# Kernel tuning notes

Measured on AMD Instinct MI355X. Metric: run time of the kernel, lower is better.

Reference implementation:

```python
import jax, jax.numpy as jnp
import numpy as np

IN_DIM = 128
HID = 128
NUM_CLASSES = 10
N_NODES = 100000
N_EDGES = 1600000
NUM_GRAPHS = 128


def setup_inputs() -> dict:
    key = jax.random.key(0)
    ks = jax.random.split(key, 12)
    X = jax.random.normal(ks[0], (N_NODES, IN_DIM), dtype=jnp.float32)
    EI = jax.random.randint(ks[1], (2, N_EDGES), 0, N_NODES, dtype=jnp.int64)
    batch = jnp.sort(jax.random.randint(ks[2], (N_NODES,), 0, NUM_GRAPHS, dtype=jnp.int64))
    s_in = 1.0 / np.sqrt(IN_DIM)
    s_h = 1.0 / np.sqrt(HID)
    s_m = 1.0 / np.sqrt(2 * HID)
    params = {
        'W1': jax.random.uniform(ks[3], (IN_DIM, HID), jnp.float32, -s_in, s_in),
        'b1': jnp.zeros((HID,), jnp.float32),
        'W2': jax.random.uniform(ks[4], (HID, HID), jnp.float32, -s_h, s_h),
        'b2': jnp.zeros((HID,), jnp.float32),
        'W3': jax.random.uniform(ks[5], (HID, HID), jnp.float32, -s_h, s_h),
        'b3': jnp.zeros((HID,), jnp.float32),
        'Wm1': jax.random.uniform(ks[6], (2 * HID, HID), jnp.float32, -s_m, s_m),
        'bm1': jnp.zeros((HID,), jnp.float32),
        'Wm2': jax.random.uniform(ks[7], (HID, NUM_CLASSES), jnp.float32, -s_h, s_h),
        'bm2': jnp.zeros((NUM_CLASSES,), jnp.float32),
    }
    return dict(X=X, EI=EI, batch=batch, num_graphs=NUM_GRAPHS, **params)


def _gcn_norm(EI, n):
    # add self loops, compute D^{-1/2}[row] * D^{-1/2}[col]
    loops = jnp.arange(n, dtype=EI.dtype)
    row = jnp.concatenate([EI[0], loops])
    col = jnp.concatenate([EI[1], loops])
    deg = jax.ops.segment_sum(jnp.ones_like(row, dtype=jnp.float32), row, num_segments=n)
    dis = (deg + 1e-12) ** -0.5
    norm = dis[row] * dis[col]
    return row, col, norm


def _gcn_layer(x, row, col, norm, W, b):
    h = x @ W + b                       # [N, out]
    msg = h[col] * norm[:, None]        # gather + scale  [E+N, out]
    return jax.ops.segment_sum(msg, row, num_segments=x.shape[0])  # scatter-add


def _pool_mean_max(x, batch, num_graphs):
    s = jax.ops.segment_sum(x, batch, num_segments=num_graphs)
    cnt = jax.ops.segment_sum(jnp.ones((x.shape[0],), x.dtype), batch, num_segments=num_graphs)
    mean = s / (cnt[:, None] + 1e-12)
    mx = jax.ops.segment_max(x, batch, num_segments=num_graphs)
    return jnp.concatenate([mean, mx], axis=1)


def reference(X, EI, batch, num_graphs, W1, b1, W2, b2, W3, b3, Wm1, bm1, Wm2, bm2):
    n = X.shape[0]
    row, col, norm = _gcn_norm(EI, n)
    x = jax.nn.relu(_gcn_layer(X, row, col, norm, W1, b1))
    x = jax.nn.relu(_gcn_layer(x, row, col, norm, W2, b2))
    x = jax.nn.relu(_gcn_layer(x, row, col, norm, W3, b3))
    g = _pool_mean_max(x, batch, num_graphs)
    h = jax.nn.relu(g @ Wm1 + bm1)
    return h @ Wm2 + bm2
```

## Files before the change

kernel.cpp:

```cpp
#include <hip/hip_runtime.h>
#include <hip/hip_fp16.h>
#include <cstdint>
#include <cstddef>

#define DIM 128
#define NG 128
#define NCLS 10
#define PSLICE 8
#define CPAD 64
#define NOWN 256
#define RPB 391
#define NPBLK 1024
#define OCAP 16
#define OVCAP 65536

typedef _Float16 f16;
typedef __attribute__((ext_vector_type(8))) _Float16 f16x8;
typedef __attribute__((ext_vector_type(4))) float f32x4;


__global__ __launch_bounds__(256) void k_part(
    const int* __restrict__ rw, const int* __restrict__ cl, int E,
    unsigned* __restrict__ buckets, int* __restrict__ bcnt,
    unsigned long long* __restrict__ ovf, int* __restrict__ ovfn) {
  __shared__ int lcnt[NOWN];
  if (threadIdx.x < NOWN) lcnt[threadIdx.x] = 0;
  __syncthreads();
  int b = blockIdx.x;
  int C = (((E + NPBLK - 1) / NPBLK + 3) & ~3);
  int s = b * C;
  int e = s + C;
  if (e > E) e = E;
  auto put = [&](int r, int c) {
    int o = (unsigned)r / RPB;
    int li = r - o * RPB;
    int sl = atomicAdd(&lcnt[o], 1);
    if (sl < OCAP) {
      buckets[((size_t)o * NPBLK + b) * OCAP + sl] =
          ((unsigned)li << 17) | (unsigned)c;
    } else {
      int oi = atomicAdd(ovfn, 1);
      if (oi < OVCAP)
        ovf[oi] = ((unsigned long long)(unsigned)r << 32) | (unsigned)c;
    }
  };
  for (int i = s + (int)threadIdx.x * 4; i < e; i += 1024) {
    if (i + 3 < e) {
      int4 r4 = *(const int4*)(rw + i);
      int4 c4 = *(const int4*)(cl + i);
      put(r4.x, c4.x);
      put(r4.y, c4.y);
      put(r4.z, c4.z);
      put(r4.w, c4.w);
    } else {
      for (int j = i; j < e; ++j) put(rw[j], cl[j]);
    }
  }
  __syncthreads();
  if (threadIdx.x < NOWN) {
    int v = lcnt[threadIdx.x];
    bcnt[threadIdx.x * NPBLK + b] = v < OCAP ? v : OCAP;
  }
}

__global__ __launch_bounds__(256) void k_place(
    const unsigned* __restrict__ buckets, const int* __restrict__ bcnt,
    const unsigned long long* __restrict__ ovf, const int* __restrict__ ovfn,
    int* __restrict__ cnt, float* __restrict__ dis, int* __restrict__ csrc,
    int N) {
  extern __shared__ int sm[];
  int* lcnt = sm;
  int* csr = sm + ((RPB + 3) & ~3);
  int o = blockIdx.x;
  int r0 = o * RPB;
  int rows = N - r0;
  if (rows > RPB) rows = RPB;
  if (rows <= 0) return;
  for (int i = threadIdx.x; i < rows; i += 256) lcnt[i] = 0;
  __syncthreads();
  const int* bc = bcnt + o * NPBLK;
  const unsigned* bp = buckets + (size_t)o * NPBLK * OCAP;
  for (int j = (int)threadIdx.x; j < NPBLK * OCAP; j += 256) {
    int seg = j >> 4;
    int pos = j & 15;
    if (pos < bc[seg]) {
      unsigned ent = bp[j];
      int li = (int)(ent >> 17);
      int c = (int)(ent & 0x1ffffu);
      int sl = atomicAdd(&lcnt[li], 1);
      if (sl < CPAD) csr[(li << 6) + sl] = c;
    }
  }
  int nov = *ovfn;
  if (nov > OVCAP) nov = OVCAP;
  for (int j = (int)threadIdx.x; j < nov; j += 256) {
    unsigned long long ent = ovf[j];
    int r = (int)(unsigned)(ent >> 32);
    int li = r - r0;
    if (li >= 0 && li < rows) {
      int c = (int)(unsigned)(ent & 0xffffffffu);
      int sl = atomicAdd(&lcnt[li], 1);
      if (sl < CPAD) csr[(li << 6) + sl] = c;
    }
  }
  __syncthreads();
  uint4* dst = (uint4*)(csrc + ((size_t)r0 << 6));
  const uint4* src = (const uint4*)csr;
  int n4 = rows * 16;
  for (int j = (int)threadIdx.x; j < n4; j += 256) dst[j] = src[j];
  for (int i = threadIdx.x; i < rows; i += 256) {
    int v = lcnt[i];
    cnt[r0 + i] = v;
    dis[r0 + i] = rsqrtf((float)(v + 1));
  }
}

__global__ void k_wt(const float* __restrict__ W1, const float* __restrict__ W2,
                     const float* __restrict__ W3, __half* __restrict__ Wt1,
                     __half* __restrict__ Wt2, __half* __restrict__ Wt3) {
  int gi = blockIdx.x * 256 + threadIdx.x;
  int m = gi / (DIM * DIM);
  int i = gi % (DIM * DIM);
  const float* W = (m == 0) ? W1 : (m == 1) ? W2 : W3;
  __half* Wt = (m == 0) ? Wt1 : (m == 1) ? Wt2 : Wt3;
  int k = i >> 7, c = i & 127;
  Wt[(size_t)c * DIM + k] = __float2half(W[(size_t)k * DIM + c]);
}


template <int FP32IN>
__global__ __launch_bounds__(256, 3) void k_gemm(
    const void* __restrict__ Ain, const __half* __restrict__ Wt,
    const float* __restrict__ bias, const float* __restrict__ dis,
    __half* __restrict__ Hh, int N) {
  int t = threadIdx.x;
  int lane = t & 63;
  int wv = t >> 6;
  int l15 = lane & 15, lg = lane >> 4;
  int cb = (wv & 1) * 64;

  f16x8 bfr[4][4];
#pragma unroll
  for (int ct = 0; ct < 4; ++ct) {
    int c = cb + ct * 16 + l15;
    const f16* wp = (const f16*)Wt + (size_t)c * DIM + lg * 8;
#pragma unroll
    for (int ks = 0; ks < 4; ++ks) bfr[ks][ct] = *(const f16x8*)(wp + ks * 32);
  }
  float bv[4];
#pragma unroll
  for (int ct = 0; ct < 4; ++ct) bv[ct] = bias[cb + ct * 16 + l15];

  const int nt2 = (N + 31) / 32;
  for (int t2 = blockIdx.x; t2 < nt2; t2 += gridDim.x) {
    int row0 = t2 * 32 + (wv >> 1) * 16;
    int rA = row0 + l15;
    if (rA > N - 1) rA = N - 1;
    f16x8 afr[4];
    if constexpr (FP32IN) {
      const float* ap = (const float*)Ain + (size_t)rA * DIM + lg * 8;
#pragma unroll
      for (int ks = 0; ks < 4; ++ks) {
        float4 v0 = *(const float4*)(ap + ks * 32);
        float4 v1 = *(const float4*)(ap + ks * 32 + 4);
        f16x8 a;
        a[0] = (f16)v0.x; a[1] = (f16)v0.y; a[2] = (f16)v0.z; a[3] = (f16)v0.w;
        a[4] = (f16)v1.x; a[5] = (f16)v1.y; a[6] = (f16)v1.z; a[7] = (f16)v1.w;
        afr[ks] = a;
      }
    } else {
      const f16* ap = (const f16*)Ain + (size_t)rA * DIM + lg * 8;
#pragma unroll
      for (int ks = 0; ks < 4; ++ks) afr[ks] = *(const f16x8*)(ap + ks * 32);
    }

    f32x4 acc[4];
#pragma unroll
    for (int ct = 0; ct < 4; ++ct) acc[ct] = (f32x4){0.f, 0.f, 0.f, 0.f};
#pragma unroll
    for (int ks = 0; ks < 4; ++ks)
#pragma unroll
      for (int ct = 0; ct < 4; ++ct)
        acc[ct] = __builtin_amdgcn_mfma_f32_16x16x32_f16(afr[ks], bfr[ks][ct], acc[ct], 0, 0, 0);

#pragma unroll
    for (int j = 0; j < 4; ++j) {
      int r = row0 + lg * 4 + j;
      if (r < N) {
        float dr = dis[r];
#pragma unroll
        for (int ct = 0; ct < 4; ++ct) {
          float o = (acc[ct][j] + bv[ct]) * dr;
          Hh[(size_t)r * DIM + cb + ct * 16 + l15] = __float2half(o);
        }
      }
    }
  }
}


__global__ __launch_bounds__(256) void k_agg(
    const __half* __restrict__ Hh, __half* __restrict__ Ah,
    const int* __restrict__ csrc, const int* __restrict__ cntA,
    const float* __restrict__ dis, int N) {
  int wave = (int)(((size_t)blockIdx.x * blockDim.x + threadIdx.x) >> 6);
  int lane = threadIdx.x & 63;
  int g = lane >> 4;
  int q = lane & 15;
  int r = wave * 4 + g;
  if (r >= N) return;
  int cnt = cntA[r];
  if (cnt > CPAD) cnt = CPAD;
  float dr = dis[r];
  const int* cp = csrc + ((size_t)r << 6);
  const f16* hb = (const f16*)Hh + q * 8;

  float4 aA0 = {0,0,0,0}, aA1 = {0,0,0,0};
  float4 aB0 = {0,0,0,0}, aB1 = {0,0,0,0};
  float4 aC0 = {0,0,0,0}, aC1 = {0,0,0,0};
  float4 aD0 = {0,0,0,0}, aD1 = {0,0,0,0};

#define ACC8(u, x0, x1)                                                   \
  {                                                                       \
    float2 f_;                                                            \
    f_ = __half22float2(*reinterpret_cast<const __half2*>(&(u).x));       \
    x0.x += f_.x; x0.y += f_.y;                                           \
    f_ = __half22float2(*reinterpret_cast<const __half2*>(&(u).y));       \
    x0.z += f_.x; x0.w += f_.y;                                           \
    f_ = __half22float2(*reinterpret_cast<const __half2*>(&(u).z));       \
    x1.x += f_.x; x1.y += f_.y;                                           \
    f_ = __half22float2(*reinterpret_cast<const __half2*>(&(u).w));       \
    x1.z += f_.x; x1.w += f_.y;                                           \
  }

  int i = 0;
  for (; i + 7 < cnt; i += 8) {
    int4 ci0 = *(const int4*)(cp + i);
    int4 ci1 = *(const int4*)(cp + i + 4);
    uint4 u0 = *(const uint4*)(hb + (size_t)ci0.x * DIM);
    uint4 u1 = *(const uint4*)(hb + (size_t)ci0.y * DIM);
    uint4 u2 = *(const uint4*)(hb + (size_t)ci0.z * DIM);
    uint4 u3 = *(const uint4*)(hb + (size_t)ci0.w * DIM);
    uint4 u4 = *(const uint4*)(hb + (size_t)ci1.x * DIM);
    uint4 u5 = *(const uint4*)(hb + (size_t)ci1.y * DIM);
    uint4 u6 = *(const uint4*)(hb + (size_t)ci1.z * DIM);
    uint4 u7 = *(const uint4*)(hb + (size_t)ci1.w * DIM);
    ACC8(u0, aA0, aA1);
    ACC8(u1, aB0, aB1);
    ACC8(u2, aC0, aC1);
    ACC8(u3, aD0, aD1);
    ACC8(u4, aA0, aA1);
    ACC8(u5, aB0, aB1);
    ACC8(u6, aC0, aC1);
    ACC8(u7, aD0, aD1);
  }
  for (; i < cnt; ++i) {
    int c0 = cp[i];
    uint4 u0 = *(const uint4*)(hb + (size_t)c0 * DIM);
    ACC8(u0, aA0, aA1);
  }
  {
    uint4 us = *(const uint4*)(hb + (size_t)r * DIM);
    ACC8(us, aA0, aA1);
  }
#undef ACC8
  float4 s0, s1;
  s0.x = (aA0.x + aB0.x) + (aC0.x + aD0.x);
  s0.y = (aA0.y + aB0.y) + (aC0.y + aD0.y);
  s0.z = (aA0.z + aB0.z) + (aC0.z + aD0.z);
  s0.w = (aA0.w + aB0.w) + (aC0.w + aD0.w);
  s1.x = (aA1.x + aB1.x) + (aC1.x + aD1.x);
  s1.y = (aA1.y + aB1.y) + (aC1.y + aD1.y);
  s1.z = (aA1.z + aB1.z) + (aC1.z + aD1.z);
  s1.w = (aA1.w + aB1.w) + (aC1.w + aD1.w);
  float o0 = fmaxf(dr * s0.x, 0.f), o1 = fmaxf(dr * s0.y, 0.f);
  float o2 = fmaxf(dr * s0.z, 0.f), o3 = fmaxf(dr * s0.w, 0.f);
  float o4 = fmaxf(dr * s1.x, 0.f), o5 = fmaxf(dr * s1.y, 0.f);
  float o6 = fmaxf(dr * s1.z, 0.f), o7 = fmaxf(dr * s1.w, 0.f);
  __half2 p0 = __floats2half2_rn(o0, o1);
  __half2 p1 = __floats2half2_rn(o2, o3);
  __half2 p2 = __floats2half2_rn(o4, o5);
  __half2 p3 = __floats2half2_rn(o6, o7);
  uint4 u;
  u.x = *(unsigned int*)&p0;
  u.y = *(unsigned int*)&p1;
  u.z = *(unsigned int*)&p2;
  u.w = *(unsigned int*)&p3;
  *(uint4*)((f16*)Ah + (size_t)r * DIM + q * 8) = u;
}


__global__ void k_bounds(const int* __restrict__ batch, int N, int G,
                         int* __restrict__ starts) {
  int i = blockIdx.x * blockDim.x + threadIdx.x;
  if (i >= N) return;
  int b = batch[i];
  int pb = (i == 0) ? -1 : batch[i - 1];
  for (int g = pb + 1; g <= b; ++g) starts[g] = i;
  if (i == N - 1) {
    for (int g = b + 1; g <= G; ++g) starts[g] = N;
  }
}

__global__ void k_pool1(const __half* __restrict__ A, const int* __restrict__ starts,
                        float* __restrict__ part) {
  int g = blockIdx.x / PSLICE, sl = blockIdx.x % PSLICE;
  int c = threadIdx.x;
  int s = starts[g], e = starts[g + 1];
  int len = e - s;
  int ns = s + (len * sl) / PSLICE;
  int ne = s + (len * (sl + 1)) / PSLICE;
  float sum = 0.f, mx = -INFINITY;
  for (int n = ns; n < ne; ++n) {
    float v = __half2float(A[(size_t)n * DIM + c]);
    sum += v;
    mx = fmaxf(mx, v);
  }
  part[((size_t)(g * PSLICE + sl) * 2 + 0) * DIM + c] = sum;
  part[((size_t)(g * PSLICE + sl) * 2 + 1) * DIM + c] = mx;
}

__global__ void k_pool2(const float* __restrict__ part, const int* __restrict__ starts,
                        float* __restrict__ GF) {
  int g = blockIdx.x;
  int c = threadIdx.x;
  float sum = 0.f, mx = -INFINITY;
  for (int sl = 0; sl < PSLICE; ++sl) {
    sum += part[((size_t)(g * PSLICE + sl) * 2 + 0) * DIM + c];
    mx = fmaxf(mx, part[((size_t)(g * PSLICE + sl) * 2 + 1) * DIM + c]);
  }
  int cntg = starts[g + 1] - starts[g];
  GF[(size_t)g * 256 + c] = sum / ((float)cntg + 1e-12f);
  GF[(size_t)g * 256 + 128 + c] = mx;
}


__global__ void k_mlp1(const float* __restrict__ GF, const float* __restrict__ Wm1,
                       const float* __restrict__ bm1, float* __restrict__ H1) {
  __shared__ float gs[256];
  int g = blockIdx.x, j = threadIdx.x;
  gs[j] = GF[(size_t)g * 256 + j];
  gs[j + 128] = GF[(size_t)g * 256 + 128 + j];
  __syncthreads();
  float acc = bm1[j];
#pragma unroll 8
  for (int k = 0; k < 256; ++k) acc = fmaf(gs[k], Wm1[k * DIM + j], acc);
  H1[(size_t)g * DIM + j] = fmaxf(acc, 0.f);
}

__global__ void k_mlp2(const float* __restrict__ H1, const float* __restrict__ Wm2,
                       const float* __restrict__ bm2, float* __restrict__ out) {
  __shared__ float hs[DIM];
  int g = blockIdx.x, j = threadIdx.x;
  hs[j] = H1[(size_t)g * DIM + j];
  hs[j + 64] = H1[(size_t)g * DIM + j + 64];
  __syncthreads();
  if (j < NCLS) {
    float acc = bm2[j];
#pragma unroll 8
    for (int k = 0; k < DIM; ++k) acc = fmaf(hs[k], Wm2[k * NCLS + j], acc);
    out[(size_t)g * NCLS + j] = acc;
  }
}


static inline size_t al256(size_t x) { return (x + 255) & ~(size_t)255; }

extern "C" void kernel_launch(void* const* d_in, const int* in_sizes, int n_in,
                              void* d_out, int out_size, void* d_ws, size_t ws_size,
                              hipStream_t stream) {
  const float* X = (const float*)d_in[0];
  const int* EI = (const int*)d_in[1];
  const int* batch = (const int*)d_in[2];
  const float* W1 = (const float*)d_in[4];
  const float* b1 = (const float*)d_in[5];
  const float* W2 = (const float*)d_in[6];
  const float* b2 = (const float*)d_in[7];
  const float* W3 = (const float*)d_in[8];
  const float* b3 = (const float*)d_in[9];
  const float* Wm1 = (const float*)d_in[10];
  const float* bm1 = (const float*)d_in[11];
  const float* Wm2 = (const float*)d_in[12];
  const float* bm2 = (const float*)d_in[13];
  float* OUT = (float*)d_out;

  const int N = in_sizes[0] / DIM;
  const int E = in_sizes[1] / 2;
  const int G = NG;

  const int* EI_row = EI;
  const int* EI_col = EI + E;

  char* p = (char*)d_ws;
  size_t off = 0;
  auto take = [&](size_t bytes) { void* r = p + off; off = al256(off + bytes); return r; };

  int* cnt = (int*)take((size_t)N * 4);
  int* bcnt = (int*)take((size_t)NOWN * NPBLK * 4);
  int* ovfn = (int*)take(256);
  unsigned long long* ovf = (unsigned long long*)take((size_t)OVCAP * 8);
  int* starts = (int*)take((size_t)(G + 1) * 4);
  float* dis = (float*)take((size_t)N * 4);
  int* csrc = (int*)take((size_t)N * CPAD * 4);
  unsigned* buckets = (unsigned*)take((size_t)NOWN * NPBLK * OCAP * 4);
  __half* Hh = (__half*)take((size_t)N * DIM * 2);
  __half* Ah = (__half*)take((size_t)N * DIM * 2);
  __half* Wt1 = (__half*)take((size_t)DIM * DIM * 2);
  __half* Wt2 = (__half*)take((size_t)DIM * DIM * 2);
  __half* Wt3 = (__half*)take((size_t)DIM * DIM * 2);
  float* part = (float*)take((size_t)G * PSLICE * 2 * DIM * 4);
  float* GF = (float*)take((size_t)G * 256 * 4);
  float* H1 = (float*)take((size_t)G * DIM * 4);
  (void)ws_size; (void)n_in; (void)out_size;

  hipMemsetAsync(ovfn, 0, 4, stream);

  k_part<<<NPBLK, 256, 0, stream>>>(EI_row, EI_col, E, buckets, bcnt, ovf, ovfn);
  const int placeLds = ((RPB + 3) & ~3) * 4 + RPB * 64 * 4;
  k_place<<<NOWN, 256, placeLds, stream>>>(buckets, bcnt, ovf, ovfn, cnt, dis, csrc, N);
  k_wt<<<192, 256, 0, stream>>>(W1, W2, W3, Wt1, Wt2, Wt3);

  const int aggBlocks = (N * 16 + 255) / 256;

  k_gemm<1><<<512, 256, 0, stream>>>(X, Wt1, b1, dis, Hh, N);
  k_agg<<<aggBlocks, 256, 0, stream>>>(Hh, Ah, csrc, cnt, dis, N);
  k_gemm<0><<<512, 256, 0, stream>>>(Ah, Wt2, b2, dis, Hh, N);
  k_agg<<<aggBlocks, 256, 0, stream>>>(Hh, Ah, csrc, cnt, dis, N);
  k_gemm<0><<<512, 256, 0, stream>>>(Ah, Wt3, b3, dis, Hh, N);
  k_agg<<<aggBlocks, 256, 0, stream>>>(Hh, Ah, csrc, cnt, dis, N);

  k_bounds<<<(N + 255) / 256, 256, 0, stream>>>(batch, N, G, starts);
  k_pool1<<<G * PSLICE, DIM, 0, stream>>>(Ah, starts, part);
  k_pool2<<<G, DIM, 0, stream>>>(part, starts, GF);

  k_mlp1<<<G, DIM, 0, stream>>>(GF, Wm1, bm1, H1);
  k_mlp2<<<G, 64, 0, stream>>>(H1, Wm2, bm2, OUT);
}
```

Measured before the change: 387.7 us.

## Split feature matrix into per-XCD column panels for L2-local aggregation

Stores the hidden feature matrices as 8 column panels of 16 halfs each. Each aggregation block reads its XCC ID from a hardware register and processes only the panel for its XCD, so each XCD's L2 caches a 3.2MB panel instead of the full matrix. Rows are taken from per-XCD atomic work counters through a persistent grid of 1024 blocks. The GEMM and pooling kernels are changed to read and write the panel layout. Correctness depends on every XCD getting enough blocks to drain its counter, and each gather is now only 8 bytes per lane, so memory transactions are narrower.

```diff
diff --git a/kernel.cpp b/kernel.cpp
--- a/kernel.cpp
+++ b/kernel.cpp
@@ -13,6 +13,8 @@
 #define NPBLK 1024
 #define OCAP 16
 #define OVCAP 65536
+#define NXCD 8
+#define XCCID_IMM ((31 << 11) | (0 << 6) | 20)
 
 typedef _Float16 f16;
 typedef __attribute__((ext_vector_type(8))) _Float16 f16x8;
@@ -132,12 +134,14 @@
 __global__ __launch_bounds__(256, 3) void k_gemm(
     const void* __restrict__ Ain, const __half* __restrict__ Wt,
     const float* __restrict__ bias, const float* __restrict__ dis,
-    __half* __restrict__ Hh, int N) {
+    __half* __restrict__ Hp, int N) {
+  const size_t PSTR = (size_t)N * 16;
   int t = threadIdx.x;
   int lane = t & 63;
   int wv = t >> 6;
   int l15 = lane & 15, lg = lane >> 4;
   int cb = (wv & 1) * 64;
+  int pb = (wv & 1) * 4;
 
   f16x8 bfr[4][4];
 #pragma unroll
@@ -169,9 +173,13 @@
         afr[ks] = a;
       }
     } else {
-      const f16* ap = (const f16*)Ain + (size_t)rA * DIM + lg * 8;
-#pragma unroll
-      for (int ks = 0; ks < 4; ++ks) afr[ks] = *(const f16x8*)(ap + ks * 32);
+      const f16* ab = (const f16*)Ain;
+      int off = (lg & 1) * 8;
+#pragma unroll
+      for (int ks = 0; ks < 4; ++ks) {
+        int p = 2 * ks + (lg >> 1);
+        afr[ks] = *(const f16x8*)(ab + (size_t)p * PSTR + (size_t)rA * 16 + off);
+      }
     }
 
     f32x4 acc[4];
@@ -191,7 +199,8 @@
 #pragma unroll
         for (int ct = 0; ct < 4; ++ct) {
           float o = (acc[ct][j] + bv[ct]) * dr;
-          Hh[(size_t)r * DIM + cb + ct * 16 + l15] = __float2half(o);
+          ((__half*)Hp)[(size_t)(pb + ct) * PSTR + (size_t)r * 16 + l15] =
+              __float2half(o);
         }
       }
     }
@@ -200,93 +209,68 @@
 
 
 __global__ __launch_bounds__(256) void k_agg(
-    const __half* __restrict__ Hh, __half* __restrict__ Ah,
+    const __half* __restrict__ Hp, __half* __restrict__ Ap,
     const int* __restrict__ csrc, const int* __restrict__ cntA,
-    const float* __restrict__ dis, int N) {
-  int wave = (int)(((size_t)blockIdx.x * blockDim.x + threadIdx.x) >> 6);
+    const float* __restrict__ dis, int N, int* __restrict__ work) {
+  __shared__ int sbase;
+  unsigned xcc = __builtin_amdgcn_s_getreg(XCCID_IMM) & (NXCD - 1);
+  const size_t PSTR = (size_t)N * 16;
+  const f16* hp = (const f16*)Hp + (size_t)xcc * PSTR;
+  f16* ap = (f16*)Ap + (size_t)xcc * PSTR;
+  int wv = threadIdx.x >> 6;
   int lane = threadIdx.x & 63;
-  int g = lane >> 4;
-  int q = lane & 15;
-  int r = wave * 4 + g;
-  if (r >= N) return;
-  int cnt = cntA[r];
-  if (cnt > CPAD) cnt = CPAD;
-  float dr = dis[r];
-  const int* cp = csrc + ((size_t)r << 6);
-  const f16* hb = (const f16*)Hh + q * 8;
-
-  float4 aA0 = {0,0,0,0}, aA1 = {0,0,0,0};
-  float4 aB0 = {0,0,0,0}, aB1 = {0,0,0,0};
-  float4 aC0 = {0,0,0,0}, aC1 = {0,0,0,0};
-  float4 aD0 = {0,0,0,0}, aD1 = {0,0,0,0};
-
-#define ACC8(u, x0, x1)                                                   \
-  {                                                                       \
-    float2 f_;                                                            \
-    f_ = __half22float2(*reinterpret_cast<const __half2*>(&(u).x));       \
-    x0.x += f_.x; x0.y += f_.y;                                           \
-    f_ = __half22float2(*reinterpret_cast<const __half2*>(&(u).y));       \
-    x0.z += f_.x; x0.w += f_.y;                                           \
-    f_ = __half22float2(*reinterpret_cast<const __half2*>(&(u).z));       \
-    x1.x += f_.x; x1.y += f_.y;                                           \
-    f_ = __half22float2(*reinterpret_cast<const __half2*>(&(u).w));       \
-    x1.z += f_.x; x1.w += f_.y;                                           \
-  }
-
-  int i = 0;
-  for (; i + 7 < cnt; i += 8) {
-    int4 ci0 = *(const int4*)(cp + i);
-    int4 ci1 = *(const int4*)(cp + i + 4);
-    uint4 u0 = *(const uint4*)(hb + (size_t)ci0.x * DIM);
-    uint4 u1 = *(const uint4*)(hb + (size_t)ci0.y * DIM);
-    uint4 u2 = *(const uint4*)(hb + (size_t)ci0.z * DIM);
-    uint4 u3 = *(const uint4*)(hb + (size_t)ci0.w * DIM);
-    uint4 u4 = *(const uint4*)(hb + (size_t)ci1.x * DIM);
-    uint4 u5 = *(const uint4*)(hb + (size_t)ci1.y * DIM);
-    uint4 u6 = *(const uint4*)(hb + (size_t)ci1.z * DIM);
-    uint4 u7 = *(const uint4*)(hb + (size_t)ci1.w * DIM);
-    ACC8(u0, aA0, aA1);
-    ACC8(u1, aB0, aB1);
-    ACC8(u2, aC0, aC1);
-    ACC8(u3, aD0, aD1);
-    ACC8(u4, aA0, aA1);
-    ACC8(u5, aB0, aB1);
-    ACC8(u6, aC0, aC1);
-    ACC8(u7, aD0, aD1);
-  }
-  for (; i < cnt; ++i) {
-    int c0 = cp[i];
-    uint4 u0 = *(const uint4*)(hb + (size_t)c0 * DIM);
-    ACC8(u0, aA0, aA1);
-  }
-  {
-    uint4 us = *(const uint4*)(hb + (size_t)r * DIM);
-    ACC8(us, aA0, aA1);
-  }
-#undef ACC8
-  float4 s0, s1;
-  s0.x = (aA0.x + aB0.x) + (aC0.x + aD0.x);
-  s0.y = (aA0.y + aB0.y) + (aC0.y + aD0.y);
-  s0.z = (aA0.z + aB0.z) + (aC0.z + aD0.z);
-  s0.w = (aA0.w + aB0.w) + (aC0.w + aD0.w);
-  s1.x = (aA1.x + aB1.x) + (aC1.x + aD1.x);
-  s1.y = (aA1.y + aB1.y) + (aC1.y + aD1.y);
-  s1.z = (aA1.z + aB1.z) + (aC1.z + aD1.z);
-  s1.w = (aA1.w + aB1.w) + (aC1.w + aD1.w);
-  float o0 = fmaxf(dr * s0.x, 0.f), o1 = fmaxf(dr * s0.y, 0.f);
-  float o2 = fmaxf(dr * s0.z, 0.f), o3 = fmaxf(dr * s0.w, 0.f);
-  float o4 = fmaxf(dr * s1.x, 0.f), o5 = fmaxf(dr * s1.y, 0.f);
-  float o6 = fmaxf(dr * s1.z, 0.f), o7 = fmaxf(dr * s1.w, 0.f);
-  __half2 p0 = __floats2half2_rn(o0, o1);
-  __half2 p1 = __floats2half2_rn(o2, o3);
-  __half2 p2 = __floats2half2_rn(o4, o5);
-  __half2 p3 = __floats2half2_rn(o6, o7);
-  uint4 u;
-  u.x = *(unsigned int*)&p0;
-  u.y = *(unsigned int*)&p1;
-  u.z = *(unsigned int*)&p2;
-  u.w = *(unsigned int*)&p3;
-  *(uint4*)((f16*)Ah + (size_t)r * DIM + q * 8) = u;
+  int rw = lane >> 2;
+  int q4 = lane & 3;
+  for (;;) {
+    if (threadIdx.x == 0) sbase = atomicAdd(&work[xcc], 64);
+    __syncthreads();
+    int base = sbase;
+    __syncthreads();
+    if (base >= N) break;
+    int r = base + wv * 16 + rw;
+    if (r < N) {
+      int cn = cntA[r];
+      if (cn > CPAD) cn = CPAD;
+      float dr = dis[r];
+      const int* cp = csrc + ((size_t)r << 6);
+      float a0 = 0.f, a1 = 0.f, a2 = 0.f, a3 = 0.f;
+      float b0 = 0.f, b1 = 0.f, b2 = 0.f, b3 = 0.f;
+      int i = 0;
+      for (; i + 1 < cn; i += 2) {
+        int c0 = cp[i], c1 = cp[i + 1];
+        uint2 u0 = *(const uint2*)(hp + (size_t)c0 * 16 + q4 * 4);
+        uint2 u1 = *(const uint2*)(hp + (size_t)c1 * 16 + q4 * 4);
+        float2 f;
+        f = __half22float2(*reinterpret_cast<__half2*>(&u0.x)); a0 += f.x; a1 += f.y;
+        f = __half22float2(*reinterpret_cast<__half2*>(&u0.y)); a2 += f.x; a3 += f.y;
+        f = __half22float2(*reinterpret_cast<__half2*>(&u1.x)); b0 += f.x; b1 += f.y;
+        f = __half22float2(*reinterpret_cast<__half2*>(&u1.y)); b2 += f.x; b3 += f.y;
+      }
+      if (i < cn) {
+        int c0 = cp[i];
+        uint2 u0 = *(const uint2*)(hp + (size_t)c0 * 16 + q4 * 4);
+        float2 f;
+        f = __half22float2(*reinterpret_cast<__half2*>(&u0.x)); a0 += f.x; a1 += f.y;
+        f = __half22float2(*reinterpret_cast<__half2*>(&u0.y)); a2 += f.x; a3 += f.y;
+      }
+      {
+        uint2 us = *(const uint2*)(hp + (size_t)r * 16 + q4 * 4);
+        float2 f;
+        f = __half22float2(*reinterpret_cast<__half2*>(&us.x)); a0 += f.x; a1 += f.y;
+        f = __half22float2(*reinterpret_cast<__half2*>(&us.y)); a2 += f.x; a3 += f.y;
+      }
+      float o0 = fmaxf(dr * (a0 + b0), 0.f);
+      float o1 = fmaxf(dr * (a1 + b1), 0.f);
+      float o2 = fmaxf(dr * (a2 + b2), 0.f);
+      float o3 = fmaxf(dr * (a3 + b3), 0.f);
+      __half2 p0 = __floats2half2_rn(o0, o1);
+      __half2 p1 = __floats2half2_rn(o2, o3);
+      uint2 u;
+      u.x = *(unsigned int*)&p0;
+      u.y = *(unsigned int*)&p1;
+      *(uint2*)(ap + (size_t)r * 16 + q4 * 4) = u;
+    }
+  }
 }
 
 
@@ -302,17 +286,19 @@
   }
 }
 
-__global__ void k_pool1(const __half* __restrict__ A, const int* __restrict__ starts,
-                        float* __restrict__ part) {
+__global__ void k_pool1(const __half* __restrict__ Ap, const int* __restrict__ starts,
+                        float* __restrict__ part, int N) {
+  const size_t PSTR = (size_t)N * 16;
   int g = blockIdx.x / PSLICE, sl = blockIdx.x % PSLICE;
   int c = threadIdx.x;
+  const __half* base = Ap + (size_t)(c >> 4) * PSTR + (c & 15);
   int s = starts[g], e = starts[g + 1];
   int len = e - s;
   int ns = s + (len * sl) / PSLICE;
   int ne = s + (len * (sl + 1)) / PSLICE;
   float sum = 0.f, mx = -INFINITY;
   for (int n = ns; n < ne; ++n) {
-    float v = __half2float(A[(size_t)n * DIM + c]);
+    float v = __half2float(base[(size_t)n * 16]);
     sum += v;
     mx = fmaxf(mx, v);
   }
@@ -398,6 +384,7 @@
   int* cnt = (int*)take((size_t)N * 4);
   int* bcnt = (int*)take((size_t)NOWN * NPBLK * 4);
   int* ovfn = (int*)take(256);
+  int* work = (int*)take((size_t)3 * NXCD * 4);
   unsigned long long* ovf = (unsigned long long*)take((size_t)OVCAP * 8);
   int* starts = (int*)take((size_t)(G + 1) * 4);
   float* dis = (float*)take((size_t)N * 4);
@@ -414,23 +401,22 @@
   (void)ws_size; (void)n_in; (void)out_size;
 
   hipMemsetAsync(ovfn, 0, 4, stream);
+  hipMemsetAsync(work, 0, (size_t)3 * NXCD * 4, stream);
 
   k_part<<<NPBLK, 256, 0, stream>>>(EI_row, EI_col, E, buckets, bcnt, ovf, ovfn);
   const int placeLds = ((RPB + 3) & ~3) * 4 + RPB * 64 * 4;
   k_place<<<NOWN, 256, placeLds, stream>>>(buckets, bcnt, ovf, ovfn, cnt, dis, csrc, N);
   k_wt<<<192, 256, 0, stream>>>(W1, W2, W3, Wt1, Wt2, Wt3);
 
-  const int aggBlocks = (N * 16 + 255) / 256;
-
   k_gemm<1><<<512, 256, 0, stream>>>(X, Wt1, b1, dis, Hh, N);
-  k_agg<<<aggBlocks, 256, 0, stream>>>(Hh, Ah, csrc, cnt, dis, N);
+  k_agg<<<1024, 256, 0, stream>>>(Hh, Ah, csrc, cnt, dis, N, work + 0);
   k_gemm<0><<<512, 256, 0, stream>>>(Ah, Wt2, b2, dis, Hh, N);
-  k_agg<<<aggBlocks, 256, 0, stream>>>(Hh, Ah, csrc, cnt, dis, N);
+  k_agg<<<1024, 256, 0, stream>>>(Hh, Ah, csrc, cnt, dis, N, work + 8);
   k_gemm<0><<<512, 256, 0, stream>>>(Ah, Wt3, b3, dis, Hh, N);
-  k_agg<<<aggBlocks, 256, 0, stream>>>(Hh, Ah, csrc, cnt, dis, N);
+  k_agg<<<1024, 256, 0, stream>>>(Hh, Ah, csrc, cnt, dis, N, work + 16);
 
   k_bounds<<<(N + 255) / 256, 256, 0, stream>>>(batch, N, G, starts);
-  k_pool1<<<G * PSLICE, DIM, 0, stream>>>(Ah, starts, part);
+  k_pool1<<<G * PSLICE, DIM, 0, stream>>>(Ah, starts, part, N);
   k_pool2<<<G, DIM, 0, stream>>>(part, starts, GF);
 
   k_mlp1<<<G, DIM, 0, stream>>>(GF, Wm1, bm1, H1);
```

Measured after the change: 704.6 us. 81.7% more time.
